# Kernel optimization log

Measured on AMD Instinct MI355X. Metric: run time of the kernel, lower is better.

Reference implementation:

```python
import jax, jax.numpy as jnp
import numpy as np

B, V, D, H, E = 512, 128, 256, 4, 2
Dh = D // H

def setup_inputs() -> dict:
    key = jax.random.key(0)
    k = jax.random.split(key, 8)
    x = jax.random.normal(k[0], (B, V, D), dtype=jnp.float32)
    adj = jax.random.randint(k[1], (V, V), 0, 2, dtype=jnp.int32)
    adj = adj.at[jnp.arange(V), jnp.arange(V)].set(1)  # self loops so no empty columns for real nodes
    edge_attr = jax.random.normal(k[2], (V, V, E), dtype=jnp.float32)
    mask = jax.random.bernoulli(k[3], 0.1, (B, V))  # True = padded view
    # learned params (torch Linear: y = x @ W.T)
    W = jax.random.normal(k[4], (D, D), dtype=jnp.float32) / np.sqrt(D)
    a = jax.random.normal(k[5], (2 * Dh,), dtype=jnp.float32) / np.sqrt(2 * Dh)  # attn.weight flattened
    Ew = jax.random.normal(k[6], (H, E), dtype=jnp.float32) / np.sqrt(E)  # edge_proj.weight
    return {"x": x, "adj": adj, "edge_attr": edge_attr, "mask": mask, "W": W, "a": a, "Ew": Ew}

def reference(x, adj, edge_attr, mask, W, a, Ew):
    Bv, Vv, Dv = x.shape
    Hh = Ew.shape[0]
    Dhh = Dv // Hh
    Wx = (x @ W.T).reshape(Bv, Vv, Hh, Dhh)                 # [B,V,H,Dh]
    a_src, a_dst = a[:Dhh], a[Dhh:]
    s_src = jnp.einsum('bvhd,d->bvh', Wx, a_src)             # a^T[Wh_i ; .]
    s_dst = jnp.einsum('bvhd,d->bvh', Wx, a_dst)             # a^T[. ; Wh_j]
    ef = jnp.einsum('ije,he->ijh', edge_attr, Ew)            # [V,V,H]
    e = s_src[:, :, None, :] + s_dst[:, None, :, :] + ef[None]  # [B,i,j,H]
    e = jnp.where(e >= 0, e, 0.2 * e)                        # leaky_relu(0.2)
    valid = (adj.astype(bool))[None, :, :, None] & (~mask)[:, :, None, None] & (~mask)[:, None, :, None]
    e = jnp.where(valid, e, -jnp.inf)
    # softmax over source dim i (axis=1), safe for all-masked columns (-> 0, like nan_to_num)
    m = jnp.max(e, axis=1, keepdims=True)
    m = jnp.where(jnp.isfinite(m), m, 0.0)
    p = jnp.where(valid, jnp.exp(e - m), 0.0)
    denom = jnp.sum(p, axis=1, keepdims=True)
    alpha = p / jnp.where(denom == 0, 1.0, denom)            # [B,i,j,H]
    h = jnp.einsum('bijh,bihd->bjhd', alpha, Wx).reshape(Bv, Vv, Dv)
    h = jax.nn.elu(h)
    return jnp.where(mask[:, :, None], 0.0, h)
```

## Files before the change

### kernel.cpp

```cpp
#include <hip/hip_runtime.h>
#include <hip/hip_bf16.h>
#include <cmath>

#define BB 512
#define VV 128
#define DD 256
#define HH 4
#define DHH 64

typedef unsigned short u16;
typedef __attribute__((ext_vector_type(8))) short bf16x8;
typedef __attribute__((ext_vector_type(4))) short bf16x4;
typedef __attribute__((ext_vector_type(4))) float f32x4;

__device__ __forceinline__ unsigned pk2(float a, float b) {
    __hip_bfloat162 h = __float22bfloat162_rn(make_float2(a, b));
    unsigned r;
    __builtin_memcpy(&r, &h, sizeof(r));
    return r;
}

__global__ __launch_bounds__(256) void k_ef(const float* __restrict__ ea,
                                            const float* __restrict__ Ew,
                                            const int* __restrict__ adj,
                                            float* __restrict__ efmT) {
    const int h = blockIdx.y;
    const int t = threadIdx.x;
    const int i = t & 127, jl = t >> 7;
    const float e0 = Ew[h * 2], e1 = Ew[h * 2 + 1];
    #pragma unroll
    for (int q = 0; q < 2; ++q) {
        const int j = blockIdx.x * 4 + q * 2 + jl;
        const int ij = i * VV + j;
        float v = -INFINITY;
        if (adj[ij]) v = fmaf(ea[ij * 2 + 1], e1, ea[ij * 2] * e0);
        efmT[((size_t)h * VV + j) * VV + i] = v;
    }
}

__global__ __launch_bounds__(256, 4) void k_fused(
    const float* __restrict__ x, const float* __restrict__ Wm,
    const float* __restrict__ a, const float* __restrict__ efmT,
    const int* __restrict__ mask, float* __restrict__ out) {
    __shared__ u16 ubuf[128 * 136];
    __shared__ float ssl[256], sdl[256], rden[2][128];
    __shared__ int mkl[128];

    u16* As  = ubuf;
    u16* Bs  = ubuf + 128 * 40;
    u16* WxL = ubuf;

    const int t = threadIdx.x;
    const int b = blockIdx.x, hp = blockIdx.y;
    const int w = t >> 6, L = t & 63;
    const int wr = w >> 1, wc = w & 1;
    const int lr = L & 15, lg = L >> 4;

    if (t < 128) mkl[t] = mask[b * VV + t];

    const int row = t >> 1, seg = t & 1;
    const float* xs = x  + ((size_t)b * VV + row) * DD + seg * 16;
    const float* ws = Wm + ((size_t)(hp * 128 + row)) * DD + seg * 16;
    u16* adst = As + row * 40 + seg * 16;
    u16* bdst = Bs + row * 40 + seg * 16;

    f32x4 acc[4][4];
    #pragma unroll
    for (int i = 0; i < 4; ++i)
        #pragma unroll
        for (int j = 0; j < 4; ++j) acc[i][j] = (f32x4){0.f, 0.f, 0.f, 0.f};

    float4 px[4], pw[4];
    #pragma unroll
    for (int q = 0; q < 4; ++q) {
        px[q] = *(const float4*)(xs + q * 4);
        pw[q] = *(const float4*)(ws + q * 4);
    }

    for (int ks = 0; ks < 8; ++ks) {
        unsigned va[4], vb[4], qa[4], qb[4];
        va[0] = pk2(px[0].x, px[0].y); va[1] = pk2(px[0].z, px[0].w);
        va[2] = pk2(px[1].x, px[1].y); va[3] = pk2(px[1].z, px[1].w);
        vb[0] = pk2(px[2].x, px[2].y); vb[1] = pk2(px[2].z, px[2].w);
        vb[2] = pk2(px[3].x, px[3].y); vb[3] = pk2(px[3].z, px[3].w);
        qa[0] = pk2(pw[0].x, pw[0].y); qa[1] = pk2(pw[0].z, pw[0].w);
        qa[2] = pk2(pw[1].x, pw[1].y); qa[3] = pk2(pw[1].z, pw[1].w);
        qb[0] = pk2(pw[2].x, pw[2].y); qb[1] = pk2(pw[2].z, pw[2].w);
        qb[2] = pk2(pw[3].x, pw[3].y); qb[3] = pk2(pw[3].z, pw[3].w);
        *(bf16x8*)adst       = *(bf16x8*)&va[0];
        *(bf16x8*)(adst + 8) = *(bf16x8*)&vb[0];
        *(bf16x8*)bdst       = *(bf16x8*)&qa[0];
        *(bf16x8*)(bdst + 8) = *(bf16x8*)&qb[0];
        __syncthreads();
        if (ks < 7) {
            #pragma unroll
            for (int q = 0; q < 4; ++q) {
                px[q] = *(const float4*)(xs + (ks + 1) * 32 + q * 4);
                pw[q] = *(const float4*)(ws + (ks + 1) * 32 + q * 4);
            }
        }
        bf16x8 af[4], bfr[4];
        #pragma unroll
        for (int mi = 0; mi < 4; ++mi)
            af[mi] = *(const bf16x8*)&As[(wr * 64 + mi * 16 + lr) * 40 + lg * 8];
        #pragma unroll
        for (int ni = 0; ni < 4; ++ni)
            bfr[ni] = *(const bf16x8*)&Bs[(wc * 64 + ni * 16 + lr) * 40 + lg * 8];
        #pragma unroll
        for (int mi = 0; mi < 4; ++mi)
            #pragma unroll
            for (int ni = 0; ni < 4; ++ni)
                acc[mi][ni] = __builtin_amdgcn_mfma_f32_16x16x32_bf16(
                    af[mi], bfr[ni], acc[mi][ni], 0, 0, 0);
        __syncthreads();
    }

    float as_[4], ad_[4];
    #pragma unroll
    for (int ni = 0; ni < 4; ++ni) {
        as_[ni] = a[ni * 16 + lr];
        ad_[ni] = a[64 + ni * 16 + lr];
    }
    float ps[16], pd[16];
    #pragma unroll
    for (int k = 0; k < 16; ++k) { ps[k] = 0.f; pd[k] = 0.f; }
    #pragma unroll
    for (int mi = 0; mi < 4; ++mi) {
        #pragma unroll
        for (int ni = 0; ni < 4; ++ni) {
            const int c  = wc * 64 + ni * 16 + lr;
            const int vb = wr * 64 + mi * 16 + lg * 4;
            unsigned o2[2];
            o2[0] = pk2(acc[mi][ni][0], acc[mi][ni][1]);
            o2[1] = pk2(acc[mi][ni][2], acc[mi][ni][3]);
            #pragma unroll
            for (int r = 0; r < 4; ++r) {
                float v = acc[mi][ni][r];
                ps[mi * 4 + r] = fmaf(v, as_[ni], ps[mi * 4 + r]);
                pd[mi * 4 + r] = fmaf(v, ad_[ni], pd[mi * 4 + r]);
            }
            *(uint2*)&WxL[c * 136 + vb] = *(uint2*)&o2[0];
        }
    }
    #pragma unroll
    for (int k = 0; k < 16; ++k) {
        #pragma unroll
        for (int m = 1; m < 16; m <<= 1) {
            ps[k] += __shfl_xor(ps[k], m);
            pd[k] += __shfl_xor(pd[k], m);
        }
    }
    if (lr == 0) {
        #pragma unroll
        for (int mi = 0; mi < 4; ++mi)
            #pragma unroll
            for (int r = 0; r < 4; ++r) {
                int v = wr * 64 + mi * 16 + lg * 4 + r;
                bool mk = mkl[v] != 0;
                ssl[wc * 128 + v] = mk ? -INFINITY : ps[mi * 4 + r];
                sdl[wc * 128 + v] = mk ? -INFINITY : pd[mi * 4 + r];
            }
    }
    __syncthreads();

    const int j0 = w * 32 + lr;
    for (int hl = 0; hl < 2; ++hl) {
        const int h = hp * 2 + hl;
        const float sdj0 = sdl[hl * 128 + j0];
        const float sdj1 = sdl[hl * 128 + j0 + 16];
        const float* ef0 = efmT + ((size_t)h * VV + j0) * VV;
        const float* ef1 = ef0 + 16 * VV;
        bf16x8 af2[2][4];
        float ps0 = 0.f, ps1 = 0.f;
        #pragma unroll
        for (int ks = 0; ks < 4; ++ks) {
            const int i0 = ks * 32 + lg * 8;
            float sv[8], ev0[8], ev1[8];
            *(float4*)&sv[0]  = *(const float4*)&ssl[hl * 128 + i0];
            *(float4*)&sv[4]  = *(const float4*)&ssl[hl * 128 + i0 + 4];
            *(float4*)&ev0[0] = *(const float4*)(ef0 + i0);
            *(float4*)&ev0[4] = *(const float4*)(ef0 + i0 + 4);
            *(float4*)&ev1[0] = *(const float4*)(ef1 + i0);
            *(float4*)&ev1[4] = *(const float4*)(ef1 + i0 + 4);
            float p0[8], p1[8];
            #pragma unroll
            for (int u = 0; u < 8; ++u) {
                float e0 = sv[u] + sdj0 + ev0[u];
                float e1 = sv[u] + sdj1 + ev1[u];
                e0 = fmaxf(e0, 0.2f * e0);
                e1 = fmaxf(e1, 0.2f * e1);
                p0[u] = __expf(e0); ps0 += p0[u];
                p1[u] = __expf(e1); ps1 += p1[u];
            }
            unsigned* a0 = (unsigned*)&af2[0][ks];
            unsigned* a1 = (unsigned*)&af2[1][ks];
            a0[0] = pk2(p0[0], p0[1]); a0[1] = pk2(p0[2], p0[3]);
            a0[2] = pk2(p0[4], p0[5]); a0[3] = pk2(p0[6], p0[7]);
            a1[0] = pk2(p1[0], p1[1]); a1[1] = pk2(p1[2], p1[3]);
            a1[2] = pk2(p1[4], p1[5]); a1[3] = pk2(p1[6], p1[7]);
        }
        ps0 += __shfl_xor(ps0, 16); ps0 += __shfl_xor(ps0, 32);
        ps1 += __shfl_xor(ps1, 16); ps1 += __shfl_xor(ps1, 32);
        if (lg == 0) {
            rden[hl][j0]      = ps0 > 0.f ? 1.f / ps0 : 0.f;
            rden[hl][j0 + 16] = ps1 > 0.f ? 1.f / ps1 : 0.f;
        }

        f32x4 acc2[2][4];
        #pragma unroll
        for (int mi = 0; mi < 2; ++mi)
            #pragma unroll
            for (int ni = 0; ni < 4; ++ni) acc2[mi][ni] = (f32x4){0.f, 0.f, 0.f, 0.f};
        #pragma unroll
        for (int ks = 0; ks < 4; ++ks) {
            const int kk = ks * 32 + lg * 8;
            #pragma unroll
            for (int ni = 0; ni < 4; ++ni) {
                bf16x8 bf2 = *(const bf16x8*)&WxL[(hl * 64 + ni * 16 + lr) * 136 + kk];
                acc2[0][ni] = __builtin_amdgcn_mfma_f32_16x16x32_bf16(
                    af2[0][ks], bf2, acc2[0][ni], 0, 0, 0);
                acc2[1][ni] = __builtin_amdgcn_mfma_f32_16x16x32_bf16(
                    af2[1][ks], bf2, acc2[1][ni], 0, 0, 0);
            }
        }
        __syncthreads();

        #pragma unroll
        for (int mi = 0; mi < 2; ++mi)
            #pragma unroll
            for (int ni = 0; ni < 4; ++ni) {
                const int dcol = ni * 16 + lr;
                const int jb   = w * 32 + mi * 16 + lg * 4;
                float* op = out + ((size_t)b * VV + jb) * DD + h * DHH + dcol;
                #pragma unroll
                for (int r = 0; r < 4; ++r) {
                    float v = acc2[mi][ni][r] * rden[hl][jb + r];
                    v = v > 0.f ? v : (__expf(v) - 1.0f);
                    op[(size_t)r * DD] = v;
                }
            }
    }
}

extern "C" void kernel_launch(void* const* d_in, const int* in_sizes, int n_in,
                              void* d_out, int out_size, void* d_ws, size_t ws_size,
                              hipStream_t stream) {
    const float* x    = (const float*)d_in[0];
    const int*   adj  = (const int*)d_in[1];
    const float* ea   = (const float*)d_in[2];
    const int*   mask = (const int*)d_in[3];
    const float* Wm   = (const float*)d_in[4];
    const float* a    = (const float*)d_in[5];
    const float* Ew   = (const float*)d_in[6];
    float* out = (float*)d_out;

    float* efmT = (float*)d_ws;

    k_ef<<<dim3(VV / 4, HH), 256, 0, stream>>>(ea, Ew, adj, efmT);
    k_fused<<<dim3(BB, 2), 256, 0, stream>>>(x, Wm, a, efmT, mask, out);
}
```

Measured before the change: 153.2 us.

## Double-buffer GEMM LDS tiles, transpose edge features via shared tile, drop barrier

The projection GEMM now uses two LDS stage buffers, so the next k-slice is converted and stored while MFMAs run on the current one, and the per-iteration trailing barrier goes away. The edge-feature kernel transposes through a padded 32x33 shared tile so its global writes are coalesced. A barrier after the second MFMA loop is removed, the mask is read straight from global memory, and the occupancy hint drops from 4 to 3 blocks per CU to make room for the larger LDS use. The costs are more shared memory per block and lower occupancy, and dropping the barrier assumes no later LDS writes conflict with reads from the previous head iteration.

Result: slower. 162.5 us (+6.0%).

```diff
diff --git a/kernel.cpp b/kernel.cpp
--- a/kernel.cpp
+++ b/kernel.cpp
@@ -10,7 +10,6 @@
 
 typedef unsigned short u16;
 typedef __attribute__((ext_vector_type(8))) short bf16x8;
-typedef __attribute__((ext_vector_type(4))) short bf16x4;
 typedef __attribute__((ext_vector_type(4))) float f32x4;
 
 __device__ __forceinline__ unsigned pk2(float a, float b) {
@@ -24,30 +23,36 @@
                                             const float* __restrict__ Ew,
                                             const int* __restrict__ adj,
                                             float* __restrict__ efmT) {
-    const int h = blockIdx.y;
+    __shared__ float tile[32][33];
+    const int jt = blockIdx.x, it = blockIdx.y, h = blockIdx.z;
     const int t = threadIdx.x;
-    const int i = t & 127, jl = t >> 7;
     const float e0 = Ew[h * 2], e1 = Ew[h * 2 + 1];
-    #pragma unroll
-    for (int q = 0; q < 2; ++q) {
-        const int j = blockIdx.x * 4 + q * 2 + jl;
+    const int jl = t & 31, il = t >> 5;
+    #pragma unroll
+    for (int p = 0; p < 4; ++p) {
+        const int i = it * 32 + p * 8 + il;
+        const int j = jt * 32 + jl;
         const int ij = i * VV + j;
         float v = -INFINITY;
         if (adj[ij]) v = fmaf(ea[ij * 2 + 1], e1, ea[ij * 2] * e0);
-        efmT[((size_t)h * VV + j) * VV + i] = v;
-    }
-}
-
-__global__ __launch_bounds__(256, 4) void k_fused(
+        tile[p * 8 + il][jl] = v;
+    }
+    __syncthreads();
+    const int i2 = t & 31, j2 = t >> 5;
+    #pragma unroll
+    for (int p = 0; p < 4; ++p) {
+        const int j = p * 8 + j2;
+        efmT[((size_t)h * VV + jt * 32 + j) * VV + it * 32 + i2] = tile[i2][j];
+    }
+}
+
+__global__ __launch_bounds__(256, 3) void k_fused(
     const float* __restrict__ x, const float* __restrict__ Wm,
     const float* __restrict__ a, const float* __restrict__ efmT,
     const int* __restrict__ mask, float* __restrict__ out) {
-    __shared__ u16 ubuf[128 * 136];
+    __shared__ u16 ubuf[20480];
     __shared__ float ssl[256], sdl[256], rden[2][128];
-    __shared__ int mkl[128];
-
-    u16* As  = ubuf;
-    u16* Bs  = ubuf + 128 * 40;
+
     u16* WxL = ubuf;
 
     const int t = threadIdx.x;
@@ -56,13 +61,10 @@
     const int wr = w >> 1, wc = w & 1;
     const int lr = L & 15, lg = L >> 4;
 
-    if (t < 128) mkl[t] = mask[b * VV + t];
-
     const int row = t >> 1, seg = t & 1;
     const float* xs = x  + ((size_t)b * VV + row) * DD + seg * 16;
     const float* ws = Wm + ((size_t)(hp * 128 + row)) * DD + seg * 16;
-    u16* adst = As + row * 40 + seg * 16;
-    u16* bdst = Bs + row * 40 + seg * 16;
+    const int dsoff = row * 40 + seg * 16;
 
     f32x4 acc[4][4];
     #pragma unroll
@@ -71,13 +73,13 @@
         for (int j = 0; j < 4; ++j) acc[i][j] = (f32x4){0.f, 0.f, 0.f, 0.f};
 
     float4 px[4], pw[4];
+
     #pragma unroll
     for (int q = 0; q < 4; ++q) {
         px[q] = *(const float4*)(xs + q * 4);
         pw[q] = *(const float4*)(ws + q * 4);
     }
-
-    for (int ks = 0; ks < 8; ++ks) {
+    {
         unsigned va[4], vb[4], qa[4], qb[4];
         va[0] = pk2(px[0].x, px[0].y); va[1] = pk2(px[0].z, px[0].w);
         va[2] = pk2(px[1].x, px[1].y); va[3] = pk2(px[1].z, px[1].w);
@@ -87,25 +89,56 @@
         qa[2] = pk2(pw[1].x, pw[1].y); qa[3] = pk2(pw[1].z, pw[1].w);
         qb[0] = pk2(pw[2].x, pw[2].y); qb[1] = pk2(pw[2].z, pw[2].w);
         qb[2] = pk2(pw[3].x, pw[3].y); qb[3] = pk2(pw[3].z, pw[3].w);
+        u16* adst = ubuf + dsoff;
+        u16* bdst = ubuf + 5120 + dsoff;
         *(bf16x8*)adst       = *(bf16x8*)&va[0];
         *(bf16x8*)(adst + 8) = *(bf16x8*)&vb[0];
         *(bf16x8*)bdst       = *(bf16x8*)&qa[0];
         *(bf16x8*)(bdst + 8) = *(bf16x8*)&qb[0];
-        __syncthreads();
+    }
+    #pragma unroll
+    for (int q = 0; q < 4; ++q) {
+        px[q] = *(const float4*)(xs + 32 + q * 4);
+        pw[q] = *(const float4*)(ws + 32 + q * 4);
+    }
+    __syncthreads();
+
+    #pragma unroll
+    for (int ks = 0; ks < 8; ++ks) {
+        const int cur = ks & 1, nxt = (ks + 1) & 1;
+        const u16* Asc = ubuf + cur * 10240;
+        const u16* Bsc = Asc + 5120;
+        bf16x8 af[4], bfr[4];
+        #pragma unroll
+        for (int mi = 0; mi < 4; ++mi)
+            af[mi] = *(const bf16x8*)&Asc[(wr * 64 + mi * 16 + lr) * 40 + lg * 8];
+        #pragma unroll
+        for (int ni = 0; ni < 4; ++ni)
+            bfr[ni] = *(const bf16x8*)&Bsc[(wc * 64 + ni * 16 + lr) * 40 + lg * 8];
         if (ks < 7) {
-            #pragma unroll
-            for (int q = 0; q < 4; ++q) {
-                px[q] = *(const float4*)(xs + (ks + 1) * 32 + q * 4);
-                pw[q] = *(const float4*)(ws + (ks + 1) * 32 + q * 4);
-            }
-        }
-        bf16x8 af[4], bfr[4];
-        #pragma unroll
-        for (int mi = 0; mi < 4; ++mi)
-            af[mi] = *(const bf16x8*)&As[(wr * 64 + mi * 16 + lr) * 40 + lg * 8];
-        #pragma unroll
-        for (int ni = 0; ni < 4; ++ni)
-            bfr[ni] = *(const bf16x8*)&Bs[(wc * 64 + ni * 16 + lr) * 40 + lg * 8];
+            unsigned va[4], vb[4], qa[4], qb[4];
+            va[0] = pk2(px[0].x, px[0].y); va[1] = pk2(px[0].z, px[0].w);
+            va[2] = pk2(px[1].x, px[1].y); va[3] = pk2(px[1].z, px[1].w);
+            vb[0] = pk2(px[2].x, px[2].y); vb[1] = pk2(px[2].z, px[2].w);
+            vb[2] = pk2(px[3].x, px[3].y); vb[3] = pk2(px[3].z, px[3].w);
+            qa[0] = pk2(pw[0].x, pw[0].y); qa[1] = pk2(pw[0].z, pw[0].w);
+            qa[2] = pk2(pw[1].x, pw[1].y); qa[3] = pk2(pw[1].z, pw[1].w);
+            qb[0] = pk2(pw[2].x, pw[2].y); qb[1] = pk2(pw[2].z, pw[2].w);
+            qb[2] = pk2(pw[3].x, pw[3].y); qb[3] = pk2(pw[3].z, pw[3].w);
+            u16* adst = ubuf + nxt * 10240 + dsoff;
+            u16* bdst = ubuf + nxt * 10240 + 5120 + dsoff;
+            *(bf16x8*)adst       = *(bf16x8*)&va[0];
+            *(bf16x8*)(adst + 8) = *(bf16x8*)&vb[0];
+            *(bf16x8*)bdst       = *(bf16x8*)&qa[0];
+            *(bf16x8*)(bdst + 8) = *(bf16x8*)&qb[0];
+            if (ks < 6) {
+                #pragma unroll
+                for (int q = 0; q < 4; ++q) {
+                    px[q] = *(const float4*)(xs + (ks + 2) * 32 + q * 4);
+                    pw[q] = *(const float4*)(ws + (ks + 2) * 32 + q * 4);
+                }
+            }
+        }
         #pragma unroll
         for (int mi = 0; mi < 4; ++mi)
             #pragma unroll
@@ -156,7 +189,7 @@
             #pragma unroll
             for (int r = 0; r < 4; ++r) {
                 int v = wr * 64 + mi * 16 + lg * 4 + r;
-                bool mk = mkl[v] != 0;
+                bool mk = mask[b * VV + v] != 0;
                 ssl[wc * 128 + v] = mk ? -INFINITY : ps[mi * 4 + r];
                 sdl[wc * 128 + v] = mk ? -INFINITY : pd[mi * 4 + r];
             }
@@ -223,7 +256,6 @@
                     af2[1][ks], bf2, acc2[1][ni], 0, 0, 0);
             }
         }
-        __syncthreads();
 
         #pragma unroll
         for (int mi = 0; mi < 2; ++mi)
@@ -256,6 +288,6 @@
 
     float* efmT = (float*)d_ws;
 
-    k_ef<<<dim3(VV / 4, HH), 256, 0, stream>>>(ea, Ew, adj, efmT);
+    k_ef<<<dim3(4, 4, HH), 256, 0, stream>>>(ea, Ew, adj, efmT);
     k_fused<<<dim3(BB, 2), 256, 0, stream>>>(x, Wm, a, efmT, mask, out);
 }
```
